# Performance work log

Hardware: AMD Instinct MI355X
Metric: run time of the kernel (lower is better)

Reference implementation:

```python
import jax, jax.numpy as jnp
import numpy as np

B, T, C = 4, 2048, 1024
N_HEADS = 16
HEAD_DIM = C // N_HEADS


def setup_inputs() -> dict:
    key = jax.random.key(0)
    k1, k2, k3 = jax.random.split(key, 3)
    x = jax.random.normal(k1, (B, T, C), dtype=jnp.float32)
    w_qkv = jax.random.normal(k2, (C, 3 * C), dtype=jnp.float32) * (1.0 / np.sqrt(C))
    w_proj = jax.random.normal(k3, (C, C), dtype=jnp.float32) * (1.0 / np.sqrt(C))
    return {"x": x, "w_qkv": w_qkv, "w_proj": w_proj}


def reference(x, w_qkv, w_proj):
    b, t, c = x.shape
    qkv = x @ w_qkv                                  # [B,T,3C]
    q, k, v = jnp.split(qkv, 3, axis=-1)
    def split_heads(u):
        return u.reshape(b, t, N_HEADS, HEAD_DIM).transpose(0, 2, 1, 3)  # [B,H,T,D]
    q, k, v = split_heads(q), split_heads(k), split_heads(v)
    scale = 1.0 / np.sqrt(HEAD_DIM)
    att = jnp.einsum('bhqd,bhkd->bhqk', q, k) * scale   # [B,H,T,T]
    causal = jnp.tril(jnp.ones((t, t), dtype=bool))
    att = jnp.where(causal[None, None], att, -jnp.inf)
    att = jax.nn.softmax(att, axis=-1)
    out = jnp.einsum('bhqk,bhkd->bhqd', att, v)         # [B,H,T,D]
    out = out.transpose(0, 2, 1, 3).reshape(b, t, c)
    return out @ w_proj
```

## Files before the change

kernel.cpp:

```cpp
#include <hip/hip_runtime.h>
#include <hip/hip_bf16.h>
#include <stdint.h>

typedef __bf16 bf16_t;
typedef __bf16 bf16x4 __attribute__((ext_vector_type(4)));
typedef __bf16 bf16x8 __attribute__((ext_vector_type(8)));
typedef float  f32x4  __attribute__((ext_vector_type(4)));

#define B_    4
#define T_    2048
#define C_    1024
#define NH    16
#define HD    64
#define M_TOT (B_ * T_)

__device__ __forceinline__ void gload16(const void* g, void* l) {
    __builtin_amdgcn_global_load_lds(
        (const __attribute__((address_space(1))) uint32_t*)g,
        (__attribute__((address_space(3))) uint32_t*)l, 16, 0, 0);
}

__global__ void conv_x_kernel(const float* __restrict__ x, bf16_t* __restrict__ xb, int n4) {
    int i = blockIdx.x * blockDim.x + threadIdx.x;
    int stride = gridDim.x * blockDim.x;
    for (; i < n4; i += stride) {
        float4 v = reinterpret_cast<const float4*>(x)[i];
        union { bf16_t h[4]; uint2 u; } p;
        p.h[0] = (bf16_t)v.x; p.h[1] = (bf16_t)v.y;
        p.h[2] = (bf16_t)v.z; p.h[3] = (bf16_t)v.w;
        reinterpret_cast<uint2*>(xb)[i] = p.u;
    }
}

__global__ void transpose_w_kernel(const float* __restrict__ w, bf16_t* __restrict__ wt,
                                   int K, int N) {
    __shared__ float tile[32][33];
    int n0 = blockIdx.x * 32, k0 = blockIdx.y * 32;
    int tx = threadIdx.x, ty = threadIdx.y;
    #pragma unroll
    for (int i = 0; i < 32; i += 8)
        tile[ty + i][tx] = w[(size_t)(k0 + ty + i) * N + n0 + tx];
    __syncthreads();
    #pragma unroll
    for (int i = 0; i < 32; i += 8)
        wt[(size_t)(n0 + ty + i) * K + k0 + tx] = (bf16_t)tile[tx][ty + i];
}

#define QSCALE 0.18033688011112042f

#define LA0 0
#define LA1 16384
#define LB0 32768
#define LB1 65536

#define GSTA(base, kt) do { int k0_ = ((kt) << 6) & (K - 1);                      \
    _Pragma("unroll") for (int c_ = 0; c_ < 2; ++c_) {                            \
        int li_ = tid + c_ * 512; int row_ = li_ >> 3;                            \
        int sw_ = (li_ & 7) ^ (row_ & 7);                                         \
        gload16(A + (size_t)(mbase + row_) * K + k0_ + sw_ * 8,                   \
                lds + (base) + li_ * 16); } } while (0)

#define GSTB(base, kt) do { int k0_ = ((kt) << 6) & (K - 1);                      \
    _Pragma("unroll") for (int c_ = 0; c_ < 4; ++c_) {                            \
        int li_ = tid + c_ * 512; int row_ = li_ >> 3;                            \
        int sw_ = (li_ & 7) ^ (row_ & 7);                                         \
        gload16(Bt + (size_t)(nbase + row_) * K + k0_ + sw_ * 8,                  \
                lds + (base) + li_ * 16); } } while (0)

#define GREAD(abase, bbase) do {                                                  \
    _Pragma("unroll") for (int mi_ = 0; mi_ < 4; ++mi_)                           \
        _Pragma("unroll") for (int kk_ = 0; kk_ < 2; ++kk_) {                     \
            int row_  = wm * 64 + mi_ * 16 + q16;                                 \
            int byte_ = (row_ * 128 + kk_ * 64 + g * 16) ^ ((row_ & 7) << 4);     \
            af[mi_ * 2 + kk_] = *reinterpret_cast<const bf16x8*>(lds + (abase) + byte_); } \
    _Pragma("unroll") for (int n_ = 0; n_ < 4; ++n_)                              \
        _Pragma("unroll") for (int kk_ = 0; kk_ < 2; ++kk_) {                     \
            int row_  = wn * 64 + n_ * 16 + q16;                                  \
            int byte_ = (row_ * 128 + kk_ * 64 + g * 16) ^ ((row_ & 7) << 4);     \
            bfr[n_ * 2 + kk_] = *reinterpret_cast<const bf16x8*>(lds + (bbase) + byte_); } } while (0)

#define GMFMA(milo) do { __builtin_amdgcn_s_setprio(1);                           \
    _Pragma("unroll") for (int mi_ = 0; mi_ < 2; ++mi_)                           \
        _Pragma("unroll") for (int kk_ = 0; kk_ < 2; ++kk_)                       \
            _Pragma("unroll") for (int n_ = 0; n_ < 4; ++n_)                      \
                acc[(milo) + mi_][n_] = __builtin_amdgcn_mfma_f32_16x16x32_bf16(  \
                    af[((milo) + mi_) * 2 + kk_], bfr[n_ * 2 + kk_],              \
                    acc[(milo) + mi_][n_], 0, 0, 0);                              \
    __builtin_amdgcn_s_setprio(0); } while (0)

template<int MODE>
__global__ __launch_bounds__(512, 2) void gemm_kernel(
    const bf16_t* __restrict__ A, const bf16_t* __restrict__ Bt,
    float* __restrict__ Cout,
    bf16_t* __restrict__ Qo, bf16_t* __restrict__ Ko, bf16_t* __restrict__ Vt,
    int M, int N, int K)
{
    __shared__ __align__(16) char lds[98304];
    const int tid  = threadIdx.x;
    const int lane = tid & 63;
    const int wid  = tid >> 6;
    const int wm   = wid >> 2, wn = wid & 3;
    const int q16  = lane & 15, g = lane >> 4;
    const int xcd = blockIdx.x & 7;
    const int i0  = blockIdx.x >> 3;
    const int mbase = (xcd * 8 + (i0 & 7)) * 128;
    const int nbase = (i0 >> 3) * 256;
    const int NITER = K >> 7;

    f32x4  acc[4][4] = {};
    bf16x8 af[8], bfr[8];

    GSTA(LA0, 0); GSTB(LB0, 0); GSTA(LA1, 1); GSTB(LB1, 1);
    asm volatile("s_waitcnt vmcnt(6)" ::: "memory");
    __builtin_amdgcn_s_barrier();
    __builtin_amdgcn_sched_barrier(0);

    #pragma unroll 1
    for (int i = 0; i < NITER; ++i) {
        GREAD(LA0, LB0);
        __builtin_amdgcn_s_barrier();
        asm volatile("s_waitcnt lgkmcnt(0)" ::: "memory");
        __builtin_amdgcn_sched_barrier(0);
        GMFMA(0);
        __builtin_amdgcn_s_barrier();
        GSTA(LA0, 2 * i + 2); GSTB(LB0, 2 * i + 2);
        __builtin_amdgcn_sched_barrier(0);
        GMFMA(2);
        asm volatile("s_waitcnt vmcnt(6)" ::: "memory");
        __builtin_amdgcn_s_barrier();
        GREAD(LA1, LB1);
        __builtin_amdgcn_s_barrier();
        asm volatile("s_waitcnt lgkmcnt(0)" ::: "memory");
        __builtin_amdgcn_sched_barrier(0);
        GMFMA(0);
        __builtin_amdgcn_s_barrier();
        GSTA(LA1, 2 * i + 3); GSTB(LB1, 2 * i + 3);
        __builtin_amdgcn_sched_barrier(0);
        GMFMA(2);
        asm volatile("s_waitcnt vmcnt(6)" ::: "memory");
        __builtin_amdgcn_s_barrier();
    }
    asm volatile("s_waitcnt vmcnt(0)" ::: "memory");

    #pragma unroll
    for (int mi = 0; mi < 4; ++mi) {
        #pragma unroll
        for (int n = 0; n < 4; ++n) {
            #pragma unroll
            for (int r = 0; r < 4; ++r) {
                int row = mbase + wm * 64 + mi * 16 + g * 4 + r;
                int col = nbase + wn * 64 + n * 16 + q16;
                float cval = acc[mi][n][r];
                if (MODE == 0) {
                    Cout[(size_t)row * N + col] = cval;
                } else {
                    int b = row >> 11, t = row & 2047;
                    int d = col & 63;
                    if (col < 1024) {
                        int h = col >> 6;
                        Qo[((size_t)(b * NH + h) * T_ + t) * HD + d] = (bf16_t)(cval * QSCALE);
                    } else if (col < 2048) {
                        int h = (col - 1024) >> 6;
                        Ko[((size_t)(b * NH + h) * T_ + t) * HD + d] = (bf16_t)cval;
                    } else {
                        int h = (col - 2048) >> 6;
                        Vt[((size_t)(b * NH + h) * HD + d) * T_ + t] = (bf16_t)cval;
                    }
                }
            }
        }
    }
}

__global__ __launch_bounds__(256, 3) void attn_kernel(
    const bf16_t* __restrict__ Q, const bf16_t* __restrict__ K,
    const bf16_t* __restrict__ Vt, bf16_t* __restrict__ out)
{
    __shared__ __align__(16) char kvbuf[2][16384];
    __shared__ __align__(16) char plds[4][4096];
    const int tid  = threadIdx.x;
    const int lane = tid & 63;
    const int wid  = tid >> 6;
    const int g    = lane >> 4;
    const int q16  = lane & 15;

    const int bid = blockIdx.x;
    const int k   = bid >> 6;
    const int bh  = bid & 63;
    const int b   = bh >> 4, h = bh & 15;
    const int qt  = (k < 4) ? (15 - k) : (k < 8) ? (k + 4) : (k < 12) ? (k - 4) : (15 - k);

    const bf16_t* Qh = Q  + (size_t)bh * T_ * HD;
    const bf16_t* Kh = K  + (size_t)bh * T_ * HD;
    const bf16_t* Vh = Vt + (size_t)bh * HD * T_;
    char* myp = plds[wid];
    const int pswz = (q16 & 7) << 4;

#define STAGE(buf, kv0) do {                                                     \
        _Pragma("unroll") for (int c = 0; c < 2; ++c) {                          \
            int li  = tid + c * 256;                                             \
            int row = li >> 3;                                                   \
            int sw  = (li & 7) ^ (row & 7);                                      \
            gload16(Kh + (size_t)((kv0) + row) * HD + sw * 8, (char*)(buf) + li * 16);          \
            gload16(Vh + (size_t)row * T_ + (kv0) + sw * 8, (char*)(buf) + 8192 + li * 16);     \
        } } while (0)

    const int nt    = 2 * qt + 2;
    const int qbase = qt * 128 + wid * 32;
    const int qg0   = qbase + q16;
    const int qg1   = qbase + 16 + q16;

    bf16x8 qf0[2], qf1[2];
    #pragma unroll
    for (int kk = 0; kk < 2; ++kk) {
        qf0[kk] = *reinterpret_cast<const bf16x8*>(Qh + (size_t)qg0 * HD + kk * 32 + g * 8);
        qf1[kk] = *reinterpret_cast<const bf16x8*>(Qh + (size_t)qg1 * HD + kk * 32 + g * 8);
    }

    f32x4 acc0[4] = {}, acc1[4] = {};
    float l0 = 0.f, l1 = 0.f;

    STAGE(kvbuf[0], 0);
    int cur = 0;
    for (int it = 0; it < nt; ++it) {
        const int kv0 = it << 6;
        if (it + 1 < nt) {
            STAGE(kvbuf[cur ^ 1], (it + 1) << 6);
            asm volatile("s_waitcnt vmcnt(4)" ::: "memory");
        } else {
            asm volatile("s_waitcnt vmcnt(0)" ::: "memory");
        }
        __builtin_amdgcn_s_barrier();
        __builtin_amdgcn_sched_barrier(0);
        const char* Kl = kvbuf[cur];
        const char* Vl = kvbuf[cur] + 8192;

        f32x4 s0[4] = {}, s1[4] = {};
        __builtin_amdgcn_s_setprio(1);
        #pragma unroll
        for (int t = 0; t < 4; ++t) {
            #pragma unroll
            for (int kk = 0; kk < 2; ++kk) {
                int row  = t * 16 + q16;
                int byte = (row * 128 + kk * 64 + g * 16) ^ ((row & 7) << 4);
                bf16x8 kf = *reinterpret_cast<const bf16x8*>(Kl + byte);
                s0[t] = __builtin_amdgcn_mfma_f32_16x16x32_bf16(kf, qf0[kk], s0[t], 0, 0, 0);
                s1[t] = __builtin_amdgcn_mfma_f32_16x16x32_bf16(kf, qf1[kk], s1[t], 0, 0, 0);
            }
        }
        __builtin_amdgcn_s_setprio(0);
        if (kv0 + 63 > qbase) {
            #pragma unroll
            for (int t = 0; t < 4; ++t)
                #pragma unroll
                for (int r = 0; r < 4; ++r) {
                    int kv = kv0 + t * 16 + g * 4 + r;
                    if (kv > qg0) s0[t][r] = -1e30f;
                    if (kv > qg1) s1[t][r] = -1e30f;
                }
        }
        #pragma unroll
        for (int t = 0; t < 4; ++t) {
            float p00 = exp2f(s0[t][0]), p01 = exp2f(s0[t][1]);
            float p02 = exp2f(s0[t][2]), p03 = exp2f(s0[t][3]);
            l0 += (p00 + p01) + (p02 + p03);
            bf16x4 pw0 = { (bf16_t)p00, (bf16_t)p01, (bf16_t)p02, (bf16_t)p03 };
            int byte = (q16 * 128 + t * 32 + g * 8) ^ pswz;
            *reinterpret_cast<bf16x4*>(myp + byte) = pw0;
            float p10 = exp2f(s1[t][0]), p11 = exp2f(s1[t][1]);
            float p12 = exp2f(s1[t][2]), p13 = exp2f(s1[t][3]);
            l1 += (p10 + p11) + (p12 + p13);
            bf16x4 pw1 = { (bf16_t)p10, (bf16_t)p11, (bf16_t)p12, (bf16_t)p13 };
            *reinterpret_cast<bf16x4*>(myp + 2048 + byte) = pw1;
        }
        asm volatile("s_waitcnt lgkmcnt(0)" ::: "memory");
        __builtin_amdgcn_sched_barrier(0);
        bf16x8 pf0[2], pf1[2];
        #pragma unroll
        for (int kk2 = 0; kk2 < 2; ++kk2) {
            int byte = (q16 * 128 + kk2 * 64 + g * 16) ^ pswz;
            pf0[kk2] = *reinterpret_cast<const bf16x8*>(myp + byte);
            pf1[kk2] = *reinterpret_cast<const bf16x8*>(myp + 2048 + byte);
        }
        __builtin_amdgcn_s_setprio(1);
        #pragma unroll
        for (int nf = 0; nf < 4; ++nf) {
            #pragma unroll
            for (int kk2 = 0; kk2 < 2; ++kk2) {
                int row  = nf * 16 + q16;
                int byte = (row * 128 + kk2 * 64 + g * 16) ^ ((row & 7) << 4);
                bf16x8 vf = *reinterpret_cast<const bf16x8*>(Vl + byte);
                acc0[nf] = __builtin_amdgcn_mfma_f32_16x16x32_bf16(vf, pf0[kk2], acc0[nf], 0, 0, 0);
                acc1[nf] = __builtin_amdgcn_mfma_f32_16x16x32_bf16(vf, pf1[kk2], acc1[nf], 0, 0, 0);
            }
        }
        __builtin_amdgcn_s_setprio(0);
        __syncthreads();
        cur ^= 1;
    }
    l0 += __shfl_xor(l0, 16, 64);
    l0 += __shfl_xor(l0, 32, 64);
    l1 += __shfl_xor(l1, 16, 64);
    l1 += __shfl_xor(l1, 32, 64);
    float inv0 = 1.f / l0, inv1 = 1.f / l1;
    #pragma unroll
    for (int nf = 0; nf < 4; ++nf) {
        bf16x4 ov0 = { (bf16_t)(acc0[nf][0] * inv0), (bf16_t)(acc0[nf][1] * inv0),
                       (bf16_t)(acc0[nf][2] * inv0), (bf16_t)(acc0[nf][3] * inv0) };
        *reinterpret_cast<bf16x4*>(
            out + (size_t)(b * T_ + qg0) * C_ + h * HD + nf * 16 + g * 4) = ov0;
        bf16x4 ov1 = { (bf16_t)(acc1[nf][0] * inv1), (bf16_t)(acc1[nf][1] * inv1),
                       (bf16_t)(acc1[nf][2] * inv1), (bf16_t)(acc1[nf][3] * inv1) };
        *reinterpret_cast<bf16x4*>(
            out + (size_t)(b * T_ + qg1) * C_ + h * HD + nf * 16 + g * 4) = ov1;
    }
#undef STAGE
}

extern "C" void kernel_launch(void* const* d_in, const int* in_sizes, int n_in,
                              void* d_out, int out_size, void* d_ws, size_t ws_size,
                              hipStream_t stream) {
    const float* x      = (const float*)d_in[0];
    const float* w_qkv  = (const float*)d_in[1];
    const float* w_proj = (const float*)d_in[2];
    float* out = (float*)d_out;

    char* ws = (char*)d_ws;
    bf16_t* xb     = (bf16_t*)(ws);
    bf16_t* wqkvT  = (bf16_t*)(ws + 16777216);
    bf16_t* wprojT = (bf16_t*)(ws + 23068672);
    bf16_t* Qb     = (bf16_t*)(ws + 25165824);
    bf16_t* Kb     = (bf16_t*)(ws + 41943040);
    bf16_t* Vtb    = (bf16_t*)(ws + 58720256);
    bf16_t* attnb  = (bf16_t*)(ws + 75497472);

    conv_x_kernel<<<2048, 256, 0, stream>>>(x, xb, (B_ * T_ * C_) / 4);
    transpose_w_kernel<<<dim3(3 * C_ / 32, C_ / 32), dim3(32, 8), 0, stream>>>(w_qkv, wqkvT, C_, 3 * C_);
    transpose_w_kernel<<<dim3(C_ / 32, C_ / 32), dim3(32, 8), 0, stream>>>(w_proj, wprojT, C_, C_);

    gemm_kernel<1><<<768, 512, 0, stream>>>(
        xb, wqkvT, nullptr, Qb, Kb, Vtb, M_TOT, 3 * C_, C_);

    attn_kernel<<<1024, 256, 0, stream>>>(Qb, Kb, Vtb, attnb);

    gemm_kernel<0><<<256, 512, 0, stream>>>(
        attnb, wprojT, out, nullptr, nullptr, nullptr, M_TOT, C_, C_);
}
```

Before: 184.5 us.

## Shrink GEMM tiles to 128x128 with 4 waves and vectorize V-transpose stores

The GEMM block tile drops from 128x256 with 8 waves to 128x128 with 4 waves, and LDS falls from 96KB to 64KB. Grid sizes double, which aims to improve occupancy and load balance across CUs. In exchange, each block reuses less data and global/L2 traffic goes up. The epilogue hoists the head and region branch out of the per-element loop and writes the transposed V output as bf16x4 vector stores instead of scalar stores.

```diff
diff --git a/kernel.cpp b/kernel.cpp
--- a/kernel.cpp
+++ b/kernel.cpp
@@ -51,20 +51,13 @@
 #define LA0 0
 #define LA1 16384
 #define LB0 32768
-#define LB1 65536
-
-#define GSTA(base, kt) do { int k0_ = ((kt) << 6) & (K - 1);                      \
-    _Pragma("unroll") for (int c_ = 0; c_ < 2; ++c_) {                            \
-        int li_ = tid + c_ * 512; int row_ = li_ >> 3;                            \
+#define LB1 49152
+
+#define GST(ptr, rbase, base, kt) do { int k0_ = ((kt) << 6) & (K - 1);           \
+    _Pragma("unroll") for (int c_ = 0; c_ < 4; ++c_) {                            \
+        int li_ = tid + c_ * 256; int row_ = li_ >> 3;                            \
         int sw_ = (li_ & 7) ^ (row_ & 7);                                         \
-        gload16(A + (size_t)(mbase + row_) * K + k0_ + sw_ * 8,                   \
-                lds + (base) + li_ * 16); } } while (0)
-
-#define GSTB(base, kt) do { int k0_ = ((kt) << 6) & (K - 1);                      \
-    _Pragma("unroll") for (int c_ = 0; c_ < 4; ++c_) {                            \
-        int li_ = tid + c_ * 512; int row_ = li_ >> 3;                            \
-        int sw_ = (li_ & 7) ^ (row_ & 7);                                         \
-        gload16(Bt + (size_t)(nbase + row_) * K + k0_ + sw_ * 8,                  \
+        gload16(ptr + (size_t)((rbase) + row_) * K + k0_ + sw_ * 8,               \
                 lds + (base) + li_ * 16); } } while (0)
 
 #define GREAD(abase, bbase) do {                                                  \
@@ -89,29 +82,30 @@
     __builtin_amdgcn_s_setprio(0); } while (0)
 
 template<int MODE>
-__global__ __launch_bounds__(512, 2) void gemm_kernel(
+__global__ __launch_bounds__(256, 2) void gemm_kernel(
     const bf16_t* __restrict__ A, const bf16_t* __restrict__ Bt,
     float* __restrict__ Cout,
     bf16_t* __restrict__ Qo, bf16_t* __restrict__ Ko, bf16_t* __restrict__ Vt,
     int M, int N, int K)
 {
-    __shared__ __align__(16) char lds[98304];
+    __shared__ __align__(16) char lds[65536];
     const int tid  = threadIdx.x;
     const int lane = tid & 63;
     const int wid  = tid >> 6;
-    const int wm   = wid >> 2, wn = wid & 3;
+    const int wm   = wid >> 1, wn = wid & 1;
     const int q16  = lane & 15, g = lane >> 4;
     const int xcd = blockIdx.x & 7;
     const int i0  = blockIdx.x >> 3;
     const int mbase = (xcd * 8 + (i0 & 7)) * 128;
-    const int nbase = (i0 >> 3) * 256;
+    const int nbase = (i0 >> 3) * 128;
     const int NITER = K >> 7;
 
     f32x4  acc[4][4] = {};
     bf16x8 af[8], bfr[8];
 
-    GSTA(LA0, 0); GSTB(LB0, 0); GSTA(LA1, 1); GSTB(LB1, 1);
-    asm volatile("s_waitcnt vmcnt(6)" ::: "memory");
+    GST(A, mbase, LA0, 0); GST(Bt, nbase, LB0, 0);
+    GST(A, mbase, LA1, 1); GST(Bt, nbase, LB1, 1);
+    asm volatile("s_waitcnt vmcnt(8)" ::: "memory");
     __builtin_amdgcn_s_barrier();
     __builtin_amdgcn_sched_barrier(0);
 
@@ -123,10 +117,10 @@
         __builtin_amdgcn_sched_barrier(0);
         GMFMA(0);
         __builtin_amdgcn_s_barrier();
-        GSTA(LA0, 2 * i + 2); GSTB(LB0, 2 * i + 2);
+        GST(A, mbase, LA0, 2 * i + 2); GST(Bt, nbase, LB0, 2 * i + 2);
         __builtin_amdgcn_sched_barrier(0);
         GMFMA(2);
-        asm volatile("s_waitcnt vmcnt(6)" ::: "memory");
+        asm volatile("s_waitcnt vmcnt(8)" ::: "memory");
         __builtin_amdgcn_s_barrier();
         GREAD(LA1, LB1);
         __builtin_amdgcn_s_barrier();
@@ -134,10 +128,10 @@
         __builtin_amdgcn_sched_barrier(0);
         GMFMA(0);
         __builtin_amdgcn_s_barrier();
-        GSTA(LA1, 2 * i + 3); GSTB(LB1, 2 * i + 3);
+        GST(A, mbase, LA1, 2 * i + 3); GST(Bt, nbase, LB1, 2 * i + 3);
         __builtin_amdgcn_sched_barrier(0);
         GMFMA(2);
-        asm volatile("s_waitcnt vmcnt(6)" ::: "memory");
+        asm volatile("s_waitcnt vmcnt(8)" ::: "memory");
         __builtin_amdgcn_s_barrier();
     }
     asm volatile("s_waitcnt vmcnt(0)" ::: "memory");
@@ -146,26 +140,32 @@
     for (int mi = 0; mi < 4; ++mi) {
         #pragma unroll
         for (int n = 0; n < 4; ++n) {
-            #pragma unroll
-            for (int r = 0; r < 4; ++r) {
-                int row = mbase + wm * 64 + mi * 16 + g * 4 + r;
-                int col = nbase + wn * 64 + n * 16 + q16;
-                float cval = acc[mi][n][r];
-                if (MODE == 0) {
-                    Cout[(size_t)row * N + col] = cval;
+            const int row0 = mbase + wm * 64 + mi * 16 + g * 4;
+            const int col0 = nbase + wn * 64 + n * 16;
+            if (MODE == 0) {
+                #pragma unroll
+                for (int r = 0; r < 4; ++r)
+                    Cout[(size_t)(row0 + r) * N + col0 + q16] = acc[mi][n][r];
+            } else {
+                const int b = row0 >> 11, t0 = row0 & 2047;
+                if (col0 < 1024) {
+                    int h = col0 >> 6, d = (col0 & 63) + q16;
+                    #pragma unroll
+                    for (int r = 0; r < 4; ++r)
+                        Qo[((size_t)(b * NH + h) * T_ + t0 + r) * HD + d] =
+                            (bf16_t)(acc[mi][n][r] * QSCALE);
+                } else if (col0 < 2048) {
+                    int h = (col0 - 1024) >> 6, d = (col0 & 63) + q16;
+                    #pragma unroll
+                    for (int r = 0; r < 4; ++r)
+                        Ko[((size_t)(b * NH + h) * T_ + t0 + r) * HD + d] =
+                            (bf16_t)acc[mi][n][r];
                 } else {
-                    int b = row >> 11, t = row & 2047;
-                    int d = col & 63;
-                    if (col < 1024) {
-                        int h = col >> 6;
-                        Qo[((size_t)(b * NH + h) * T_ + t) * HD + d] = (bf16_t)(cval * QSCALE);
-                    } else if (col < 2048) {
-                        int h = (col - 1024) >> 6;
-                        Ko[((size_t)(b * NH + h) * T_ + t) * HD + d] = (bf16_t)cval;
-                    } else {
-                        int h = (col - 2048) >> 6;
-                        Vt[((size_t)(b * NH + h) * HD + d) * T_ + t] = (bf16_t)cval;
-                    }
+                    int h = (col0 - 2048) >> 6, d = (col0 & 63) + q16;
+                    bf16x4 vv = { (bf16_t)acc[mi][n][0], (bf16_t)acc[mi][n][1],
+                                  (bf16_t)acc[mi][n][2], (bf16_t)acc[mi][n][3] };
+                    *reinterpret_cast<bf16x4*>(
+                        Vt + ((size_t)(b * NH + h) * HD + d) * T_ + t0) = vv;
                 }
             }
         }
@@ -338,11 +338,11 @@
     transpose_w_kernel<<<dim3(3 * C_ / 32, C_ / 32), dim3(32, 8), 0, stream>>>(w_qkv, wqkvT, C_, 3 * C_);
     transpose_w_kernel<<<dim3(C_ / 32, C_ / 32), dim3(32, 8), 0, stream>>>(w_proj, wprojT, C_, C_);
 
-    gemm_kernel<1><<<768, 512, 0, stream>>>(
+    gemm_kernel<1><<<1536, 256, 0, stream>>>(
         xb, wqkvT, nullptr, Qb, Kb, Vtb, M_TOT, 3 * C_, C_);
 
     attn_kernel<<<1024, 256, 0, stream>>>(Qb, Kb, Vtb, attnb);
 
-    gemm_kernel<0><<<256, 512, 0, stream>>>(
+    gemm_kernel<0><<<512, 256, 0, stream>>>(
         attnb, wprojT, out, nullptr, nullptr, nullptr, M_TOT, C_, C_);
 }
```

Result: faster. 164.2 us (-11.0%).
